# Kernel tuning notes

Hardware: AMD Instinct MI355X
Metric: run time of the kernel (lower is better)

## Reference

```python
import jax, jax.numpy as jnp
import numpy as np

N, E, F = 50000, 800000, 64
GIN_F, H1, H2, OUT = 32, 128, 256, 2


def _lin_init(key, fan_in, fan_out):
    return jax.random.normal(key, (fan_in, fan_out), dtype=jnp.float32) / np.float32(np.sqrt(fan_in))


def setup_inputs() -> dict:
    key = jax.random.key(0)
    ks = jax.random.split(key, 24)
    inp = {
        "x": jax.random.normal(ks[0], (N, F), dtype=jnp.float32),
        "edge_index": jax.random.randint(ks[1], (2, E), 0, N, dtype=jnp.int64),
    }
    # GIN: 3 GINConv layers, each MLP = Linear->ReLU->Linear, then output Linear
    dims = [GIN_F, H1, H1]
    k = 2
    for i, din in enumerate(dims):
        inp[f"g{i}_w1"] = _lin_init(ks[k], din, H1); k += 1
        inp[f"g{i}_b1"] = jnp.zeros((H1,), jnp.float32)
        inp[f"g{i}_w2"] = _lin_init(ks[k], H1, H1); k += 1
        inp[f"g{i}_b2"] = jnp.zeros((H1,), jnp.float32)
    inp["gout_w"] = _lin_init(ks[k], H1, H1); k += 1
    inp["gout_b"] = jnp.zeros((H1,), jnp.float32)
    # SAGE: 2 SAGEConv layers (mean aggregation)
    sdims = [(F + H1, H2), (H2, OUT)]
    for i, (din, dout) in enumerate(sdims):
        inp[f"s{i}_wl"] = _lin_init(ks[k], din, dout); k += 1
        inp[f"s{i}_wr"] = _lin_init(ks[k], din, dout); k += 1
        inp[f"s{i}_b"] = jnp.zeros((dout,), jnp.float32)
    return inp


def _agg_sum(h, src, dst, n):
    # gather messages at src, scatter-add into dst: [N, d]
    return jax.ops.segment_sum(h[src], dst, num_segments=n)


def _forward(x, edge_index, g0_w1, g0_b1, g0_w2, g0_b2, g1_w1, g1_b1, g1_w2, g1_b2,
             g2_w1, g2_b1, g2_w2, g2_b2, gout_w, gout_b,
             s0_wl, s0_wr, s0_b, s1_wl, s1_wr, s1_b):
    src, dst = edge_index[0], edge_index[1]
    n = x.shape[0]
    deg = jax.ops.segment_sum(jnp.ones((src.shape[0],), x.dtype), dst, num_segments=n)
    inv_deg = (1.0 / jnp.maximum(deg, 1.0))[:, None]  # [N,1]

    # GIN branch on selected features (indices 0..31)
    h = x[:, :GIN_F]
    for w1, b1, w2, b2 in ((g0_w1, g0_b1, g0_w2, g0_b2),
                           (g1_w1, g1_b1, g1_w2, g1_b2),
                           (g2_w1, g2_b1, g2_w2, g2_b2)):
        m = h + _agg_sum(h, src, dst, n)        # (1+eps)*x + sum_neigh, eps=0
        h = jax.nn.relu(jax.nn.relu(m @ w1 + b1) @ w2 + b2)
    gin_out = h @ gout_w + gout_b               # [N, H1]

    # concat raw features with GIN embedding
    h = jnp.concatenate([x, gin_out], axis=1)   # [N, F+H1]

    # SAGE branch (mean aggregation)
    mean1 = _agg_sum(h, src, dst, n) * inv_deg
    h = jax.nn.relu(h @ s0_wl + mean1 @ s0_wr + s0_b)
    mean2 = _agg_sum(h, src, dst, n) * inv_deg
    out = h @ s1_wl + mean2 @ s1_wr + s1_b      # [N, OUT]
    return out


def reference(x, edge_index, g0_w1, g0_b1, g0_w2, g0_b2, g1_w1, g1_b1, g1_w2, g1_b2,
              g2_w1, g2_b1, g2_w2, g2_b2, gout_w, gout_b,
              s0_wl, s0_wr, s0_b, s1_wl, s1_wr, s1_b):
    return _forward(x, edge_index, g0_w1, g0_b1, g0_w2, g0_b2, g1_w1, g1_b1, g1_w2, g1_b2,
                    g2_w1, g2_b1, g2_w2, g2_b2, gout_w, gout_b,
                    s0_wl, s0_wr, s0_b, s1_wl, s1_wr, s1_b)
```

## Files before the change

kernel.cpp:

```cpp
#include <hip/hip_runtime.h>


typedef unsigned short ushort_t;
typedef __bf16 bf16x8 __attribute__((ext_vector_type(8)));
typedef float f32x4 __attribute__((ext_vector_type(4)));

__device__ __forceinline__ float b2f(unsigned int u16) {
    union { unsigned int i; float f; } v;
    v.i = u16 << 16;
    return v.f;
}
__device__ __forceinline__ unsigned short f2b(float f) {
    union { float f; unsigned int i; } v;
    v.f = f;
    unsigned int x = v.i;
    unsigned int r = (x + 0x7fffu + ((x >> 16) & 1u)) >> 16;
    return (unsigned short)r;
}

__global__ void detect_kernel(const int* __restrict__ ei, int ncheck, int* flag) {
    int t = blockIdx.x * blockDim.x + threadIdx.x;
    if (t < ncheck) {
        if (ei[2 * t + 1] != 0) atomicAnd(flag, 0);
    }
}

__global__ void deg_kernel(const int* __restrict__ ei, int E, const int* __restrict__ flag,
                           int* __restrict__ deg) {
    int e = blockIdx.x * blockDim.x + threadIdx.x;
    if (e >= E) return;
    int d = (*flag) ? ei[2 * ((size_t)E + e)] : ei[(size_t)E + e];
    atomicAdd(&deg[d], 1);
}

__global__ __launch_bounds__(256) void scanA_kernel(const int* __restrict__ deg, int n,
                                                    int* __restrict__ rowptr,
                                                    int* __restrict__ blocksum) {
    __shared__ int sh[256];
    int b = blockIdx.x, tid = threadIdx.x;
    int base = b * 2048 + tid * 8;
    int v[8];
#pragma unroll
    for (int e = 0; e < 8; ++e) {
        int i = base + e;
        v[e] = (i < n) ? deg[i] : 0;
    }
    int t = 0;
#pragma unroll
    for (int e = 0; e < 8; ++e) { int x = v[e]; v[e] = t; t += x; }
    sh[tid] = t;
    __syncthreads();
    for (int off = 1; off < 256; off <<= 1) {
        int val = (tid >= off) ? sh[tid - off] : 0;
        __syncthreads();
        sh[tid] += val;
        __syncthreads();
    }
    int excl = sh[tid] - t;
#pragma unroll
    for (int e = 0; e < 8; ++e) {
        int i = base + e;
        if (i < n) rowptr[i] = excl + v[e];
    }
    if (tid == 255) blocksum[b] = sh[255];
}

__global__ __launch_bounds__(256) void scanB_kernel(const int* __restrict__ blocksum, int nb,
                                                    int* __restrict__ blockoff,
                                                    int* __restrict__ rowptr, int n) {
    __shared__ int sh[256];
    int tid = threadIdx.x;
    int v = (tid < nb) ? blocksum[tid] : 0;
    sh[tid] = v;
    __syncthreads();
    for (int off = 1; off < 256; off <<= 1) {
        int t = (tid >= off) ? sh[tid - off] : 0;
        __syncthreads();
        sh[tid] += t;
        __syncthreads();
    }
    if (tid < nb) blockoff[tid] = sh[tid] - v;
    if (tid == 255) rowptr[n] = sh[255];
}

__global__ void scanC_kernel(const int* __restrict__ deg, int n, const int* __restrict__ blockoff,
                             int* __restrict__ rowptr, float* __restrict__ invdeg,
                             float* __restrict__ mask) {
    int i = blockIdx.x * blockDim.x + threadIdx.x;
    if (i >= n) return;
    rowptr[i] = rowptr[i] + blockoff[i >> 11];
    int d = deg[i];
    invdeg[i] = 1.0f / fmaxf((float)d, 1.0f);
    mask[i] = (d > 0) ? 1.0f : 0.0f;
}

__global__ void bucketinit_kernel(const int* __restrict__ rowptr, int Nn, int nbkt,
                                  int* __restrict__ bucket_cursor) {
    int b = blockIdx.x * blockDim.x + threadIdx.x;
    if (b < nbkt) bucket_cursor[b] = rowptr[min(b << 8, Nn)];
}

__global__ __launch_bounds__(256) void binA_kernel(
    const int* __restrict__ ei, int E, const int* __restrict__ flag,
    int* __restrict__ bucket_cursor, unsigned* __restrict__ stage) {
    __shared__ unsigned sPair[4096];
    __shared__ int cnt[256], off[256], gst[256];
    int tid = threadIdx.x;
    cnt[tid] = 0;
    __syncthreads();
    int base = blockIdx.x * 4096;
    bool i64 = (*flag) != 0;
    unsigned u[16];
    int bk[16];
#pragma unroll
    for (int k = 0; k < 16; ++k) {
        int e = base + tid + k * 256;
        if (e < E) {
            int s_, d_;
            if (i64) { s_ = ei[2 * (size_t)e]; d_ = ei[2 * ((size_t)E + e)]; }
            else     { s_ = ei[e];             d_ = ei[(size_t)E + e]; }
            bk[k] = d_ >> 8;
            u[k] = (unsigned)s_ | ((unsigned)(d_ & 255) << 16) | ((unsigned)bk[k] << 24);
            atomicAdd(&cnt[bk[k]], 1);
        } else bk[k] = -1;
    }
    __syncthreads();
    int c = cnt[tid];
    off[tid] = c;
    __syncthreads();
    for (int o = 1; o < 256; o <<= 1) {
        int v = (tid >= o) ? off[tid - o] : 0;
        __syncthreads();
        off[tid] += v;
        __syncthreads();
    }
    int incl = off[tid];
    __syncthreads();
    off[tid] = incl - c;
    __syncthreads();
#pragma unroll
    for (int k = 0; k < 16; ++k) {
        if (bk[k] >= 0) {
            int p = atomicAdd(&off[bk[k]], 1);
            sPair[p] = u[k];
        }
    }
    if (c > 0) gst[tid] = atomicAdd(&bucket_cursor[tid], c);
    __syncthreads();
    int total = off[255];
    for (int idx = tid; idx < total; idx += 256) {
        unsigned v = sPair[idx];
        int b = (int)(v >> 24);
        int bstart = off[b] - cnt[b];
        stage[gst[b] + (idx - bstart)] = v;
    }
}

__global__ __launch_bounds__(256) void binB_kernel(
    const unsigned* __restrict__ stage, const int* __restrict__ rowptr,
    int Nn, int* __restrict__ col) {
    __shared__ int curs[256];
    int b = blockIdx.x, tid = threadIdx.x;
    int n0 = b << 8;
    if (n0 + tid < Nn) curs[tid] = rowptr[n0 + tid];
    __syncthreads();
    int s = rowptr[n0];
    int e = rowptr[min(n0 + 256, Nn)];
    for (int i = s + tid; i < e; i += 256) {
        unsigned u = stage[i];
        int p = atomicAdd(&curs[(u >> 16) & 255], 1);
        col[p] = (int)(u & 0xffffu);
    }
}

__global__ void xconv_kernel(const float* __restrict__ x, ushort_t* __restrict__ xb, int total16) {
    int idx = blockIdx.x * blockDim.x + threadIdx.x;
    if (idx >= total16) return;
    float4 v = *(const float4*)&x[(size_t)idx * 4];
    ushort4 u;
    u.x = f2b(v.x); u.y = f2b(v.y); u.z = f2b(v.z); u.w = f2b(v.w);
    *(ushort4*)&xb[(size_t)idx * 4] = u;
}

__global__ void foldw_kernel(const float* __restrict__ gw, const float* __restrict__ gb,
                             const float* __restrict__ s0wl, const float* __restrict__ s0wr,
                             const float* __restrict__ s0bias,
                             float* __restrict__ Fl, float* __restrict__ Fr,
                             float* __restrict__ bias2, float* __restrict__ cvec) {
    int idx = blockIdx.x * blockDim.x + threadIdx.x;
    if (idx >= 128 * 256) return;
    int k = idx >> 8, n = idx & 255;
    const float* wl = s0wl + 64 * 256;
    const float* wr = s0wr + 64 * 256;
    float al = 0.f, ar = 0.f;
    for (int j = 0; j < 128; ++j) {
        float g = gw[k * 128 + j];
        al += g * wl[j * 256 + n];
        ar += g * wr[j * 256 + n];
    }
    Fl[k * 256 + n] = al;
    Fr[k * 256 + n] = ar;
    if (k == 0) {
        float bl = 0.f, br = 0.f;
        for (int j = 0; j < 128; ++j) {
            float g = gb[j];
            bl += g * wl[j * 256 + n];
            br += g * wr[j * 256 + n];
        }
        bias2[n] = s0bias[n] + bl;
        cvec[n] = br;
    }
}

struct WtDesc { const float* src; ushort_t* dst; int lk2; int K; int N; int base; };
struct WtArgs { WtDesc d[10]; int total; };
__global__ void wtconv_kernel(WtArgs a) {
    int idx = blockIdx.x * blockDim.x + threadIdx.x;
    if (idx >= a.total) return;
    int s = 0;
#pragma unroll
    for (int i = 1; i < 10; ++i) if (idx >= a.d[i].base) s = i;
    int local = idx - a.d[s].base;
    int K = a.d[s].K;
    int n = local >> a.d[s].lk2;
    int k = local & (K - 1);
    unsigned off = (unsigned)((n >> 4) * (K >> 5) + (k >> 5)) * 512u
                 + (unsigned)(((n & 15) | (((k >> 3) & 3) << 4)) << 3) + (unsigned)(k & 7);
    a.d[s].dst[off] = f2b(a.d[s].src[(size_t)k * a.d[s].N + n]);
}

template <int VEC>
__device__ __forceinline__ void ldrow(const ushort_t* p, float* t) {
    if constexpr (VEC == 1) {
        t[0] = b2f(p[0]);
    } else if constexpr (VEC == 2) {
        unsigned int v = *(const unsigned int*)p;
        t[0] = b2f(v & 0xffffu); t[1] = b2f(v >> 16);
    } else {
        uint2 v = *(const uint2*)p;
        t[0] = b2f(v.x & 0xffffu); t[1] = b2f(v.x >> 16);
        t[2] = b2f(v.y & 0xffffu); t[3] = b2f(v.y >> 16);
    }
}

template <int VEC, int MODE>
__global__ __launch_bounds__(256) void aggb_kernel(
    const ushort_t* __restrict__ h, int ldh,
    const int* __restrict__ rowptr, const int* __restrict__ col,
    const float* __restrict__ invdeg,
    ushort_t* __restrict__ out, int ldo, int Nn, int lanes) {
    int wid = blockIdx.x * 4 + ((int)threadIdx.x >> 6);
    int lane = (int)threadIdx.x & 63;
    if (wid >= Nn || lane >= lanes) return;

    const ushort_t* hb = h + (size_t)lane * VEC;
    float a[VEC];
#pragma unroll
    for (int v = 0; v < VEC; ++v) a[v] = 0.f;

    int p0 = rowptr[wid], p1 = rowptr[wid + 1];
    int p = p0;
    for (; p + 4 <= p1; p += 4) {
        int j0 = col[p], j1 = col[p + 1], j2 = col[p + 2], j3 = col[p + 3];
        float t0[VEC], t1[VEC], t2[VEC], t3[VEC];
        ldrow<VEC>(hb + (size_t)j0 * ldh, t0);
        ldrow<VEC>(hb + (size_t)j1 * ldh, t1);
        ldrow<VEC>(hb + (size_t)j2 * ldh, t2);
        ldrow<VEC>(hb + (size_t)j3 * ldh, t3);
#pragma unroll
        for (int v = 0; v < VEC; ++v) a[v] += (t0[v] + t1[v]) + (t2[v] + t3[v]);
    }
    for (; p < p1; ++p) {
        float t[VEC];
        ldrow<VEC>(hb + (size_t)col[p] * ldh, t);
#pragma unroll
        for (int v = 0; v < VEC; ++v) a[v] += t[v];
    }

    if constexpr (MODE == 0) {
        float t[VEC];
        ldrow<VEC>(hb + (size_t)wid * ldh, t);
#pragma unroll
        for (int v = 0; v < VEC; ++v) a[v] += t[v];
    } else {
        float s = invdeg[wid];
#pragma unroll
        for (int v = 0; v < VEC; ++v) a[v] *= s;
    }

    ushort_t* op = out + (size_t)wid * ldo + (size_t)lane * VEC;
    if constexpr (VEC == 1) {
        op[0] = f2b(a[0]);
    } else if constexpr (VEC == 2) {
        unsigned int v = (unsigned int)f2b(a[0]) | ((unsigned int)f2b(a[1]) << 16);
        *(unsigned int*)op = v;
    } else {
        uint2 v;
        v.x = (unsigned int)f2b(a[0]) | ((unsigned int)f2b(a[1]) << 16);
        v.y = (unsigned int)f2b(a[2]) | ((unsigned int)f2b(a[3]) << 16);
        *(uint2*)op = v;
    }
}

__global__ __launch_bounds__(256) void aggdual_kernel(
    const ushort_t* __restrict__ xb,
    const int* __restrict__ rowptr, const int* __restrict__ col,
    const float* __restrict__ invdeg,
    ushort_t* __restrict__ out32, ushort_t* __restrict__ out64, int Nn) {
    int wid = blockIdx.x * 4 + ((int)threadIdx.x >> 6);
    int lane = (int)threadIdx.x & 63;
    if (wid >= Nn) return;
    const ushort_t* hb = xb + lane;
    float a = 0.f;
    int p = rowptr[wid], p1 = rowptr[wid + 1];
    for (; p + 4 <= p1; p += 4) {
        float v0 = b2f(hb[(size_t)col[p] * 64]);
        float v1 = b2f(hb[(size_t)col[p + 1] * 64]);
        float v2 = b2f(hb[(size_t)col[p + 2] * 64]);
        float v3 = b2f(hb[(size_t)col[p + 3] * 64]);
        a += (v0 + v1) + (v2 + v3);
    }
    for (; p < p1; ++p) a += b2f(hb[(size_t)col[p] * 64]);
    out64[(size_t)wid * 64 + lane] = f2b(a * invdeg[wid]);
    if (lane < 32) {
        float self = b2f(hb[(size_t)wid * 64]);
        out32[(size_t)wid * 32 + lane] = f2b(a + self);
    }
}

struct GPass { const ushort_t* A; const ushort_t* Wp; int lda; int K; };
struct FArgs {
    GPass p[4]; int np;
    const ushort_t* W2p; const ushort_t* W3p;
    const float* b1; const float* b2; const float* b3;
    int relu1, relu2, relu3;
    int chain;
    const float* rowmask; const float* cvec;
};

__global__ __launch_bounds__(512) void fgemm_kernel(
    FArgs fa, int M, ushort_t* __restrict__ out, int ldc) {
    __shared__ __align__(16) ushort_t Tlds[4 * 64 * 40];

    int rowbase = blockIdx.x * 64;
    int colbase = blockIdx.y * 128;
    int tid = threadIdx.x;
    int lane = tid & 63, wid = tid >> 6;
    int wr3 = wid & 3, wc2 = wid >> 2;
    int lr = lane & 15, lk = (lane >> 4) * 8, rq = (lane >> 4) * 4;

    f32x4 acc[4];
#pragma unroll
    for (int j = 0; j < 4; ++j) acc[j] = (f32x4){0.f, 0.f, 0.f, 0.f};

    for (int q = 0; q < fa.np; ++q) {
        const ushort_t* A = fa.p[q].A;
        const ushort_t* Wp = fa.p[q].Wp;
        int lda = fa.p[q].lda, K = fa.p[q].K;
        int nch = K >> 5;
        for (int u = tid; u < 256 * nch; u += 512) {
            int c = u >> 8, r = (u >> 2) & 63, seg = u & 3;
            int gr = rowbase + r;
            uint4 va = make_uint4(0u, 0u, 0u, 0u);
            if (gr < M) va = *(const uint4*)&A[(size_t)gr * lda + c * 32 + seg * 8];
            *(uint4*)&Tlds[c * 2560 + r * 40 + seg * 8] = va;
        }
        __syncthreads();
        int cg0 = (colbase >> 4) + wc2 * 4;
        for (int c = 0; c < nch; ++c) {
            bf16x8 af = *(const bf16x8*)&Tlds[c * 2560 + (wr3 * 16 + lr) * 40 + lk];
            bf16x8 bfr[4];
#pragma unroll
            for (int j = 0; j < 4; ++j)
                bfr[j] = *(const bf16x8*)&Wp[((size_t)(cg0 + j) * nch + c) * 512 + lane * 8];
#pragma unroll
            for (int j = 0; j < 4; ++j)
                acc[j] = __builtin_amdgcn_mfma_f32_16x16x32_bf16(af, bfr[j], acc[j], 0, 0, 0);
        }
        __syncthreads();
    }

    for (int g = 2; g <= fa.chain; ++g) {
        const float* bprev = (g == 2) ? fa.b1 : fa.b2;
        int reluprev = (g == 2) ? fa.relu1 : fa.relu2;
        const ushort_t* Wp = (g == 2) ? fa.W2p : fa.W3p;
#pragma unroll
        for (int j = 0; j < 4; ++j) {
            int colj = wc2 * 64 + j * 16 + lr;
            float bv = bprev[colj];
#pragma unroll
            for (int t = 0; t < 4; ++t) {
                int row = wr3 * 16 + rq + t;
                float v = acc[j][t] + bv;
                if (reluprev) v = fmaxf(v, 0.f);
                Tlds[(colj >> 5) * 2560 + row * 40 + (colj & 31)] = f2b(v);
            }
            acc[j] = (f32x4){0.f, 0.f, 0.f, 0.f};
        }
        __syncthreads();
        int cg0 = wc2 * 4;
        for (int c = 0; c < 4; ++c) {
            bf16x8 af = *(const bf16x8*)&Tlds[c * 2560 + (wr3 * 16 + lr) * 40 + lk];
            bf16x8 bfr[4];
#pragma unroll
            for (int j = 0; j < 4; ++j)
                bfr[j] = *(const bf16x8*)&Wp[((size_t)(cg0 + j) * 4 + c) * 512 + lane * 8];
#pragma unroll
            for (int j = 0; j < 4; ++j)
                acc[j] = __builtin_amdgcn_mfma_f32_16x16x32_bf16(af, bfr[j], acc[j], 0, 0, 0);
        }
        __syncthreads();
    }

    const float* bf_ = (fa.chain == 1) ? fa.b1 : (fa.chain == 2) ? fa.b2 : fa.b3;
    int reluf = (fa.chain == 1) ? fa.relu1 : (fa.chain == 2) ? fa.relu2 : fa.relu3;
    float rm[4];
#pragma unroll
    for (int t = 0; t < 4; ++t) {
        int gr = rowbase + wr3 * 16 + rq + t;
        rm[t] = (fa.cvec && gr < M) ? fa.rowmask[gr] : 0.f;
    }
#pragma unroll
    for (int j = 0; j < 4; ++j) {
        int colj = wc2 * 64 + j * 16 + lr;
        float bv = bf_[colbase + colj];
        float cv = fa.cvec ? fa.cvec[colbase + colj] : 0.f;
#pragma unroll
        for (int t = 0; t < 4; ++t) {
            int row = wr3 * 16 + rq + t;
            float v = acc[j][t] + bv + rm[t] * cv;
            if (reluf) v = fmaxf(v, 0.f);
            Tlds[row * 128 + colj] = f2b(v);
        }
    }
    __syncthreads();
    for (int u = tid; u < 1024; u += 512) {
        int row = u >> 4, seg = u & 15;
        int gr = rowbase + row;
        if (gr < M)
            *(uint4*)&out[(size_t)gr * ldc + colbase + seg * 8] =
                *(const uint4*)&Tlds[row * 128 + seg * 8];
    }
}

__global__ void zproj_kernel(const ushort_t* __restrict__ s0,
                             const float* __restrict__ wl, const float* __restrict__ wr,
                             float2* __restrict__ zl, float2* __restrict__ z, int M) {
    int wave = threadIdx.x >> 6;
    int lane = threadIdx.x & 63;
    int i = blockIdx.x * 4 + wave;
    if (i >= M) return;
    float l0 = 0.f, l1 = 0.f, r0 = 0.f, r1 = 0.f;
    for (int k = lane; k < 256; k += 64) {
        float hv = b2f(s0[(size_t)i * 256 + k]);
        float2 wlv = *(const float2*)&wl[2 * k];
        float2 wrv = *(const float2*)&wr[2 * k];
        l0 += hv * wlv.x; l1 += hv * wlv.y;
        r0 += hv * wrv.x; r1 += hv * wrv.y;
    }
#pragma unroll
    for (int off = 32; off > 0; off >>= 1) {
        l0 += __shfl_down(l0, off);
        l1 += __shfl_down(l1, off);
        r0 += __shfl_down(r0, off);
        r1 += __shfl_down(r1, off);
    }
    if (lane == 0) {
        zl[i] = make_float2(l0, l1);
        z[i] = make_float2(r0, r1);
    }
}

__global__ void aggz_kernel(const float2* __restrict__ z, const float2* __restrict__ zl,
                            const int* __restrict__ rowptr, const int* __restrict__ col,
                            const float* __restrict__ invdeg, const float* __restrict__ b,
                            float* __restrict__ out, int Nn) {
    int i = blockIdx.x * blockDim.x + threadIdx.x;
    if (i >= Nn) return;
    float s0 = 0.f, s1 = 0.f;
    int p = rowptr[i], p1 = rowptr[i + 1];
    for (; p + 4 <= p1; p += 4) {
        float2 a = z[col[p]], c = z[col[p + 1]], d = z[col[p + 2]], e = z[col[p + 3]];
        s0 += (a.x + c.x) + (d.x + e.x);
        s1 += (a.y + c.y) + (d.y + e.y);
    }
    for (; p < p1; ++p) {
        float2 a = z[col[p]];
        s0 += a.x; s1 += a.y;
    }
    float inv = invdeg[i];
    float2 l = zl[i];
    out[(size_t)i * 2 + 0] = l.x + inv * s0 + b[0];
    out[(size_t)i * 2 + 1] = l.y + inv * s1 + b[1];
}

extern "C" void kernel_launch(void* const* d_in, const int* in_sizes, int n_in,
                              void* d_out, int out_size, void* d_ws, size_t ws_size,
                              hipStream_t stream) {
    const float* x      = (const float*)d_in[0];
    const int*   ei     = (const int*)d_in[1];
    const float* g_w1[3] = {(const float*)d_in[2], (const float*)d_in[6],  (const float*)d_in[10]};
    const float* g_b1[3] = {(const float*)d_in[3], (const float*)d_in[7],  (const float*)d_in[11]};
    const float* g_w2[3] = {(const float*)d_in[4], (const float*)d_in[8],  (const float*)d_in[12]};
    const float* g_b2[3] = {(const float*)d_in[5], (const float*)d_in[9],  (const float*)d_in[13]};
    const float* gout_w = (const float*)d_in[14];
    const float* gout_b = (const float*)d_in[15];
    const float* s0_wl  = (const float*)d_in[16];
    const float* s0_wr  = (const float*)d_in[17];
    const float* s0_b   = (const float*)d_in[18];
    const float* s1_wl  = (const float*)d_in[19];
    const float* s1_wr  = (const float*)d_in[20];
    const float* s1_b   = (const float*)d_in[21];
    float* out = (float*)d_out;

    const int N = in_sizes[0] / 64;
    const int E = in_sizes[1] / 2;

    char* ws = (char*)d_ws;
    size_t o = 0;
    auto take = [&](size_t bytes) -> char* {
        char* p = ws + o;
        o = (o + bytes + 255) & ~(size_t)255;
        return p;
    };
    ushort_t* xb     = (ushort_t*)take((size_t)N * 64 * 2);
    ushort_t* bA     = (ushort_t*)take((size_t)N * 128 * 2);
    ushort_t* bB     = (ushort_t*)take((size_t)N * 128 * 2);
    ushort_t* bC     = (ushort_t*)take((size_t)N * 128 * 2);
    ushort_t* aggxb  = (ushort_t*)take((size_t)N * 64 * 2);
    ushort_t* agggb  = (ushort_t*)take((size_t)N * 128 * 2);
    ushort_t* s0b    = (ushort_t*)take((size_t)N * 256 * 2);
    float2*   zlb    = (float2*)take((size_t)N * 2 * 4);
    float2*   zb     = (float2*)take((size_t)N * 2 * 4);
    float* Flbuf = (float*)take(128 * 256 * 4);
    float* Frbuf = (float*)take(128 * 256 * 4);
    float* bias2 = (float*)take(256 * 4);
    float* cvecb = (float*)take(256 * 4);
    ushort_t* w1t0 = (ushort_t*)take(128 * 32 * 2);
    ushort_t* w2t0 = (ushort_t*)take(128 * 128 * 2);
    ushort_t* w1t1 = (ushort_t*)take(128 * 128 * 2);
    ushort_t* w2t1 = (ushort_t*)take(128 * 128 * 2);
    ushort_t* w1t2 = (ushort_t*)take(128 * 128 * 2);
    ushort_t* w2t2 = (ushort_t*)take(128 * 128 * 2);
    ushort_t* wltop = (ushort_t*)take(256 * 64 * 2);
    ushort_t* wglp  = (ushort_t*)take(256 * 128 * 2);
    ushort_t* wrtop = (ushort_t*)take(256 * 64 * 2);
    ushort_t* wgrp  = (ushort_t*)take(256 * 128 * 2);
    unsigned* stage  = (unsigned*)take((size_t)E * 4);
    int*   colI   = (int*)take((size_t)E * 4);
    int*   rowptr = (int*)take((size_t)(N + 1) * 4);
    int*   deg    = (int*)take((size_t)N * 4);
    float* invdeg = (float*)take((size_t)N * 4);
    float* maskb  = (float*)take((size_t)N * 4);
    int*   blocksum = (int*)take(256 * 4);
    int*   blockoff = (int*)take(256 * 4);
    int*   bucket_cursor = (int*)take(512 * 4);
    int*   flag   = (int*)take(4);

    hipMemsetAsync(deg, 0, (size_t)N * 4, stream);
    hipMemsetAsync(flag, 1, 4, stream);

    const int TB = 256;
    const int nb = (N + 2047) / 2048;
    const int NBKT = (N + 255) >> 8;

    detect_kernel<<<4, TB, 0, stream>>>(ei, 1024, flag);
    deg_kernel<<<(E + TB - 1) / TB, TB, 0, stream>>>(ei, E, flag, deg);
    scanA_kernel<<<nb, 256, 0, stream>>>(deg, N, rowptr, blocksum);
    scanB_kernel<<<1, 256, 0, stream>>>(blocksum, nb, blockoff, rowptr, N);
    scanC_kernel<<<(N + TB - 1) / TB, TB, 0, stream>>>(deg, N, blockoff, rowptr, invdeg, maskb);
    bucketinit_kernel<<<(NBKT + 255) / 256, 256, 0, stream>>>(rowptr, N, NBKT, bucket_cursor);
    binA_kernel<<<(E + 4095) / 4096, 256, 0, stream>>>(ei, E, flag, bucket_cursor, stage);
    binB_kernel<<<NBKT, 256, 0, stream>>>(stage, rowptr, N, colI);

    foldw_kernel<<<128, 256, 0, stream>>>(gout_w, gout_b, s0_wl, s0_wr, s0_b,
                                          Flbuf, Frbuf, bias2, cvecb);
    WtArgs wa;
    const float* wsrc[10] = {g_w1[0], g_w2[0], g_w1[1], g_w2[1], g_w1[2], g_w2[2],
                             s0_wl, Flbuf, s0_wr, Frbuf};
    ushort_t* wdst[10]    = {w1t0, w2t0, w1t1, w2t1, w1t2, w2t2,
                             wltop, wglp, wrtop, wgrp};
    int wk[10]  = {32, 128, 128, 128, 128, 128, 64, 128, 64, 128};
    int wl2[10] = {5, 7, 7, 7, 7, 7, 6, 7, 6, 7};
    int wn[10]  = {128, 128, 128, 128, 128, 128, 256, 256, 256, 256};
    int base = 0;
    for (int i = 0; i < 10; ++i) {
        wa.d[i].src = wsrc[i]; wa.d[i].dst = wdst[i];
        wa.d[i].lk2 = wl2[i]; wa.d[i].K = wk[i]; wa.d[i].N = wn[i]; wa.d[i].base = base;
        base += wk[i] * wn[i];
    }
    wa.total = base;
    wtconv_kernel<<<(base + TB - 1) / TB, TB, 0, stream>>>(wa);

    xconv_kernel<<<((N * 16) + TB - 1) / TB, TB, 0, stream>>>(x, xb, N * 16);

    const int AGG_GRID = (N + 3) / 4;
    const int GX = (N + 63) / 64;

    aggdual_kernel<<<AGG_GRID, 256, 0, stream>>>(xb, rowptr, colI, invdeg, bB, aggxb, N);

    {
        FArgs fa = {};
        fa.p[0] = {bB, w1t0, 32, 32};
        fa.np = 1;
        fa.W2p = w2t0;
        fa.b1 = g_b1[0]; fa.b2 = g_b2[0];
        fa.relu1 = 1; fa.relu2 = 1;
        fa.chain = 2;
        fgemm_kernel<<<dim3(GX, 1), 512, 0, stream>>>(fa, N, bA, 128);
    }

    aggb_kernel<2, 0><<<AGG_GRID, 256, 0, stream>>>(bA, 128, rowptr, colI, invdeg, bB, 128, N, 64);
    {
        FArgs fa = {};
        fa.p[0] = {bB, w1t1, 128, 128};
        fa.np = 1;
        fa.W2p = w2t1;
        fa.b1 = g_b1[1]; fa.b2 = g_b2[1];
        fa.relu1 = 1; fa.relu2 = 1;
        fa.chain = 2;
        fgemm_kernel<<<dim3(GX, 1), 512, 0, stream>>>(fa, N, bC, 128);
    }

    aggb_kernel<2, 0><<<AGG_GRID, 256, 0, stream>>>(bC, 128, rowptr, colI, invdeg, bB, 128, N, 64);
    {
        FArgs fa = {};
        fa.p[0] = {bB, w1t2, 128, 128};
        fa.np = 1;
        fa.W2p = w2t2;
        fa.b1 = g_b1[2]; fa.b2 = g_b2[2];
        fa.relu1 = 1; fa.relu2 = 1;
        fa.chain = 2;
        fgemm_kernel<<<dim3(GX, 1), 512, 0, stream>>>(fa, N, bA, 128);
    }

    aggb_kernel<2, 1><<<AGG_GRID, 256, 0, stream>>>(bA, 128, rowptr, colI, invdeg, agggb, 128, N, 64);

    {
        FArgs fa = {};
        fa.p[0] = {xb, wltop, 64, 64};
        fa.p[1] = {bA, wglp, 128, 128};
        fa.p[2] = {aggxb, wrtop, 64, 64};
        fa.p[3] = {agggb, wgrp, 128, 128};
        fa.np = 4;
        fa.b1 = bias2;
        fa.relu1 = 1;
        fa.chain = 1;
        fa.rowmask = maskb; fa.cvec = cvecb;
        fgemm_kernel<<<dim3(GX, 2), 512, 0, stream>>>(fa, N, s0b, 256);
    }

    zproj_kernel<<<(N + 3) / 4, 256, 0, stream>>>(s0b, s1_wl, s1_wr, zlb, zb, N);
    aggz_kernel<<<(N + TB - 1) / TB, TB, 0, stream>>>(zb, zlb, rowptr, colI, invdeg, s1_b, out, N);
}
```

Before: 364.2 us.

## Split 128-wide aggregation into two 64-column passes, unroll GEMM passes, fold bucket init

Each 128-column neighbour aggregation now runs as two launches over 64-column halves, using a one-element-per-lane template instead of two per lane. The goal is a smaller per-pass working set and better cache hit rate on the gathered rows. The GEMM K-loop is templated on chunk count so it fully unrolls. Bucket cursor initialisation moves into the scan kernel, removing one launch. The split doubles the reads of the CSR indices and adds launches.

```diff
diff --git a/kernel.cpp b/kernel.cpp
--- a/kernel.cpp
+++ b/kernel.cpp
@@ -85,19 +85,15 @@
 
 __global__ void scanC_kernel(const int* __restrict__ deg, int n, const int* __restrict__ blockoff,
                              int* __restrict__ rowptr, float* __restrict__ invdeg,
-                             float* __restrict__ mask) {
+                             float* __restrict__ mask, int* __restrict__ bucket_cursor) {
     int i = blockIdx.x * blockDim.x + threadIdx.x;
     if (i >= n) return;
-    rowptr[i] = rowptr[i] + blockoff[i >> 11];
+    int r = rowptr[i] + blockoff[i >> 11];
+    rowptr[i] = r;
+    if ((i & 255) == 0) bucket_cursor[i >> 8] = r;
     int d = deg[i];
     invdeg[i] = 1.0f / fmaxf((float)d, 1.0f);
     mask[i] = (d > 0) ? 1.0f : 0.0f;
-}
-
-__global__ void bucketinit_kernel(const int* __restrict__ rowptr, int Nn, int nbkt,
-                                  int* __restrict__ bucket_cursor) {
-    int b = blockIdx.x * blockDim.x + threadIdx.x;
-    if (b < nbkt) bucket_cursor[b] = rowptr[min(b << 8, Nn)];
 }
 
 __global__ __launch_bounds__(256) void binA_kernel(
@@ -338,6 +334,38 @@
     const float* rowmask; const float* cvec;
 };
 
+template <int NCH>
+__device__ __forceinline__ void fg_pass(
+    const ushort_t* __restrict__ A, const ushort_t* __restrict__ Wp, int lda,
+    int rowbase, int colbase, int M, ushort_t* Tlds, f32x4 (&acc)[4],
+    int tid, int lane, int wr3, int wc2, int lr, int lk) {
+#pragma unroll
+    for (int u0 = 0; u0 < NCH * 256; u0 += 512) {
+        int u = tid + u0;
+        if (u < NCH * 256) {
+            int c = u >> 8, r = (u >> 2) & 63, seg = u & 3;
+            int gr = rowbase + r;
+            uint4 va = make_uint4(0u, 0u, 0u, 0u);
+            if (gr < M) va = *(const uint4*)&A[(size_t)gr * lda + c * 32 + seg * 8];
+            *(uint4*)&Tlds[c * 2560 + r * 40 + seg * 8] = va;
+        }
+    }
+    __syncthreads();
+    int cg0 = (colbase >> 4) + wc2 * 4;
+#pragma unroll
+    for (int c = 0; c < NCH; ++c) {
+        bf16x8 af = *(const bf16x8*)&Tlds[c * 2560 + (wr3 * 16 + lr) * 40 + lk];
+        bf16x8 bfr[4];
+#pragma unroll
+        for (int j = 0; j < 4; ++j)
+            bfr[j] = *(const bf16x8*)&Wp[((size_t)(cg0 + j) * NCH + c) * 512 + lane * 8];
+#pragma unroll
+        for (int j = 0; j < 4; ++j)
+            acc[j] = __builtin_amdgcn_mfma_f32_16x16x32_bf16(af, bfr[j], acc[j], 0, 0, 0);
+    }
+    __syncthreads();
+}
+
 __global__ __launch_bounds__(512) void fgemm_kernel(
     FArgs fa, int M, ushort_t* __restrict__ out, int ldc) {
     __shared__ __align__(16) ushort_t Tlds[4 * 64 * 40];
@@ -356,28 +384,12 @@
     for (int q = 0; q < fa.np; ++q) {
         const ushort_t* A = fa.p[q].A;
         const ushort_t* Wp = fa.p[q].Wp;
-        int lda = fa.p[q].lda, K = fa.p[q].K;
-        int nch = K >> 5;
-        for (int u = tid; u < 256 * nch; u += 512) {
-            int c = u >> 8, r = (u >> 2) & 63, seg = u & 3;
-            int gr = rowbase + r;
-            uint4 va = make_uint4(0u, 0u, 0u, 0u);
-            if (gr < M) va = *(const uint4*)&A[(size_t)gr * lda + c * 32 + seg * 8];
-            *(uint4*)&Tlds[c * 2560 + r * 40 + seg * 8] = va;
-        }
-        __syncthreads();
-        int cg0 = (colbase >> 4) + wc2 * 4;
-        for (int c = 0; c < nch; ++c) {
-            bf16x8 af = *(const bf16x8*)&Tlds[c * 2560 + (wr3 * 16 + lr) * 40 + lk];
-            bf16x8 bfr[4];
-#pragma unroll
-            for (int j = 0; j < 4; ++j)
-                bfr[j] = *(const bf16x8*)&Wp[((size_t)(cg0 + j) * nch + c) * 512 + lane * 8];
-#pragma unroll
-            for (int j = 0; j < 4; ++j)
-                acc[j] = __builtin_amdgcn_mfma_f32_16x16x32_bf16(af, bfr[j], acc[j], 0, 0, 0);
-        }
-        __syncthreads();
+        int lda = fa.p[q].lda;
+        switch (fa.p[q].K >> 5) {
+            case 1: fg_pass<1>(A, Wp, lda, rowbase, colbase, M, Tlds, acc, tid, lane, wr3, wc2, lr, lk); break;
+            case 2: fg_pass<2>(A, Wp, lda, rowbase, colbase, M, Tlds, acc, tid, lane, wr3, wc2, lr, lk); break;
+            default: fg_pass<4>(A, Wp, lda, rowbase, colbase, M, Tlds, acc, tid, lane, wr3, wc2, lr, lk); break;
+        }
     }
 
     for (int g = 2; g <= fa.chain; ++g) {
@@ -399,6 +411,7 @@
         }
         __syncthreads();
         int cg0 = wc2 * 4;
+#pragma unroll
         for (int c = 0; c < 4; ++c) {
             bf16x8 af = *(const bf16x8*)&Tlds[c * 2560 + (wr3 * 16 + lr) * 40 + lk];
             bf16x8 bfr[4];
@@ -568,8 +581,7 @@
     deg_kernel<<<(E + TB - 1) / TB, TB, 0, stream>>>(ei, E, flag, deg);
     scanA_kernel<<<nb, 256, 0, stream>>>(deg, N, rowptr, blocksum);
     scanB_kernel<<<1, 256, 0, stream>>>(blocksum, nb, blockoff, rowptr, N);
-    scanC_kernel<<<(N + TB - 1) / TB, TB, 0, stream>>>(deg, N, blockoff, rowptr, invdeg, maskb);
-    bucketinit_kernel<<<(NBKT + 255) / 256, 256, 0, stream>>>(rowptr, N, NBKT, bucket_cursor);
+    scanC_kernel<<<(N + TB - 1) / TB, TB, 0, stream>>>(deg, N, blockoff, rowptr, invdeg, maskb, bucket_cursor);
     binA_kernel<<<(E + 4095) / 4096, 256, 0, stream>>>(ei, E, flag, bucket_cursor, stage);
     binB_kernel<<<NBKT, 256, 0, stream>>>(stage, rowptr, N, colI);
 
@@ -597,6 +609,16 @@
     const int AGG_GRID = (N + 3) / 4;
     const int GX = (N + 63) / 64;
 
+    auto agg128 = [&](const ushort_t* src, ushort_t* dst, int mode) {
+        if (mode == 0) {
+            aggb_kernel<1, 0><<<AGG_GRID, 256, 0, stream>>>(src, 128, rowptr, colI, invdeg, dst, 128, N, 64);
+            aggb_kernel<1, 0><<<AGG_GRID, 256, 0, stream>>>(src + 64, 128, rowptr, colI, invdeg, dst + 64, 128, N, 64);
+        } else {
+            aggb_kernel<1, 1><<<AGG_GRID, 256, 0, stream>>>(src, 128, rowptr, colI, invdeg, dst, 128, N, 64);
+            aggb_kernel<1, 1><<<AGG_GRID, 256, 0, stream>>>(src + 64, 128, rowptr, colI, invdeg, dst + 64, 128, N, 64);
+        }
+    };
+
     aggdual_kernel<<<AGG_GRID, 256, 0, stream>>>(xb, rowptr, colI, invdeg, bB, aggxb, N);
 
     {
@@ -610,7 +632,7 @@
         fgemm_kernel<<<dim3(GX, 1), 512, 0, stream>>>(fa, N, bA, 128);
     }
 
-    aggb_kernel<2, 0><<<AGG_GRID, 256, 0, stream>>>(bA, 128, rowptr, colI, invdeg, bB, 128, N, 64);
+    agg128(bA, bB, 0);
     {
         FArgs fa = {};
         fa.p[0] = {bB, w1t1, 128, 128};
@@ -622,7 +644,7 @@
         fgemm_kernel<<<dim3(GX, 1), 512, 0, stream>>>(fa, N, bC, 128);
     }
 
-    aggb_kernel<2, 0><<<AGG_GRID, 256, 0, stream>>>(bC, 128, rowptr, colI, invdeg, bB, 128, N, 64);
+    agg128(bC, bB, 0);
     {
         FArgs fa = {};
         fa.p[0] = {bB, w1t2, 128, 128};
@@ -634,7 +656,7 @@
         fgemm_kernel<<<dim3(GX, 1), 512, 0, stream>>>(fa, N, bA, 128);
     }
 
-    aggb_kernel<2, 1><<<AGG_GRID, 256, 0, stream>>>(bA, 128, rowptr, colI, invdeg, agggb, 128, N, 64);
+    agg128(bA, agggb, 1);
 
     {
         FArgs fa = {};
```

Result: slower. 467.4 us (+28.3%).
